# Performance work log

Measured on AMD Instinct MI355X. Metric: run time of the kernel, lower is better.

The kernel has to match this reference:

```python
import jax, jax.numpy as jnp
import numpy as np

H = 32        # query heads
KVH = 8       # kv heads
HD = 64       # head_dim
N_REP = H // KVH
THETA = 10000.0


def _rope_cos_sin(seq_len, dim):
    # freqs_cis[t, i] = exp(1j * t * theta^{-2i/dim}) -> return cos, sin [S, dim//2]
    inv_freq = 1.0 / (THETA ** (jnp.arange(0, dim, 2, dtype=jnp.float32) / dim))
    t = jnp.arange(seq_len, dtype=jnp.float32)
    freqs = jnp.outer(t, inv_freq)  # [S, dim//2]
    return jnp.cos(freqs), jnp.sin(freqs)


def _apply_rope(x, cos, sin):
    # x: [B, S, h, HD]; pairs are interleaved (even=real, odd=imag)
    xr = x[..., 0::2]
    xi = x[..., 1::2]
    c = cos[None, :, None, :]
    s = sin[None, :, None, :]
    out_r = xr * c - xi * s
    out_i = xr * s + xi * c
    return jnp.stack([out_r, out_i], axis=-1).reshape(x.shape)


def setup_inputs() -> dict:
    key = jax.random.key(0)
    ks = jax.random.split(key, 5)
    D = 2048
    B, S = 1, 2048
    scale = 0.02
    return {
        "hidden_states": jax.random.normal(ks[0], (B, S, D), jnp.float32),
        "Wq": jax.random.normal(ks[1], (D, H * HD), jnp.float32) * scale,
        "Wk": jax.random.normal(ks[2], (D, KVH * HD), jnp.float32) * scale,
        "Wv": jax.random.normal(ks[3], (D, KVH * HD), jnp.float32) * scale,
        "Wo": jax.random.normal(ks[4], (H * HD, D), jnp.float32) * scale,
    }


def reference(hidden_states, Wq, Wk, Wv, Wo):
    B, S, D = hidden_states.shape
    xq = (hidden_states @ Wq).reshape(B, S, H, HD)
    xk = (hidden_states @ Wk).reshape(B, S, KVH, HD)
    xv = (hidden_states @ Wv).reshape(B, S, KVH, HD)

    cos, sin = _rope_cos_sin(S, HD)
    xq = _apply_rope(xq, cos, sin)
    xk = _apply_rope(xk, cos, sin)

    # GQA: expand kv heads (kv head g -> query heads g*N_REP .. g*N_REP+N_REP-1)
    keys = jnp.repeat(xk, N_REP, axis=2)    # [B, S, H, HD]
    values = jnp.repeat(xv, N_REP, axis=2)

    q = xq.transpose(0, 2, 1, 3)      # [B, H, S, HD]
    k = keys.transpose(0, 2, 1, 3)
    v = values.transpose(0, 2, 1, 3)

    scores = jnp.einsum('bhqd,bhkd->bhqk', q, k) / jnp.sqrt(jnp.float32(HD))
    causal = jnp.tril(jnp.ones((S, S), dtype=bool))
    scores = jnp.where(causal[None, None], scores, jnp.float32(-jnp.inf))
    probs = jax.nn.softmax(scores.astype(jnp.float32), axis=-1).astype(q.dtype)

    out = jnp.einsum('bhqk,bhkd->bhqd', probs, v)   # [B, H, S, HD]
    out = out.transpose(0, 2, 1, 3).reshape(B, S, H * HD)
    return out @ Wo
```

## Files before the change

kernel.cpp:

```cpp
#include <hip/hip_runtime.h>


#define NH  32
#define NKV 8

typedef __attribute__((ext_vector_type(8))) __bf16 bf16x8;
typedef __attribute__((ext_vector_type(4))) float  f32x4;

#define SCALE_LOG2 0.18033688011112042f
#define L2_10K_32  0.41524101186098665f

__device__ __forceinline__ void glds16(const __bf16* g, __bf16* l) {
  __builtin_amdgcn_global_load_lds(
      (const __attribute__((address_space(1))) unsigned int*)g,
      (__attribute__((address_space(3))) unsigned int*)l, 16, 0, 0);
}

__device__ __forceinline__ float qmax16(float v) {
  int t;
  t = __builtin_amdgcn_mov_dpp(__builtin_bit_cast(int, v), 0x128, 0xf, 0xf, true);
  v = fmaxf(v, __builtin_bit_cast(float, t));
  t = __builtin_amdgcn_mov_dpp(__builtin_bit_cast(int, v), 0x124, 0xf, 0xf, true);
  v = fmaxf(v, __builtin_bit_cast(float, t));
  t = __builtin_amdgcn_mov_dpp(__builtin_bit_cast(int, v), 0x122, 0xf, 0xf, true);
  v = fmaxf(v, __builtin_bit_cast(float, t));
  t = __builtin_amdgcn_mov_dpp(__builtin_bit_cast(int, v), 0x121, 0xf, 0xf, true);
  v = fmaxf(v, __builtin_bit_cast(float, t));
  return v;
}

__device__ __forceinline__ float pair_swap(float v) {
  int t = __builtin_amdgcn_mov_dpp(__builtin_bit_cast(int, v), 0xB1, 0xf, 0xf, true);
  return __builtin_bit_cast(float, t);
}

__device__ __forceinline__ unsigned pack_bf16(float lo, float hi) {
  union { __bf16 b[2]; unsigned u; } r;
  r.b[0] = (__bf16)lo; r.b[1] = (__bf16)hi;
  return r.u;
}

__global__ void k_prep(const float* __restrict__ hx, const float* __restrict__ Wq,
                       const float* __restrict__ Wk, const float* __restrict__ Wv,
                       const float* __restrict__ Wo, __bf16* __restrict__ Xb,
                       __bf16* __restrict__ Wqkvt, __bf16* __restrict__ Wot) {
  __shared__ float t[32][33];
  const int nt = blockIdx.x, k0 = blockIdx.y * 32;
  const int tx = threadIdx.x, ty = threadIdx.y;
  if (nt >= 160) {
    int c0 = (nt - 160) * 32;
#pragma unroll
    for (int j = 0; j < 4; j++) {
      size_t idx = (size_t)(k0 + ty + j * 8) * 2048 + c0 + tx;
      Xb[idx] = (__bf16)hx[idx];
    }
    return;
  }
  const float* W; int ldW, n0; __bf16* dst;
  if (nt < 64)      { W = Wq; ldW = 2048; dst = Wqkvt;                        n0 = nt * 32; }
  else if (nt < 80) { W = Wk; ldW = 512;  dst = Wqkvt + (size_t)2048 * 2048;  n0 = (nt - 64) * 32; }
  else if (nt < 96) { W = Wv; ldW = 512;  dst = Wqkvt + (size_t)2560 * 2048;  n0 = (nt - 80) * 32; }
  else              { W = Wo; ldW = 2048; dst = Wot;                          n0 = (nt - 96) * 32; }
#pragma unroll
  for (int j = 0; j < 4; j++)
    t[ty + j * 8][tx] = W[(size_t)(k0 + ty + j * 8) * ldW + n0 + tx];
  __syncthreads();
#pragma unroll
  for (int j = 0; j < 4; j++)
    dst[(size_t)(n0 + ty + j * 8) * 2048 + k0 + tx] = (__bf16)t[tx][ty + j * 8];
}

__global__ void k_vtrans_b(const __bf16* __restrict__ V, __bf16* __restrict__ Vt) {
  __shared__ __bf16 t[32][33];
  int c0 = blockIdx.x * 32, s0 = blockIdx.y * 32;
  int tx = threadIdx.x, ty = threadIdx.y;
#pragma unroll
  for (int j = 0; j < 4; j++)
    t[ty + j * 8][tx] = V[(size_t)(s0 + ty + j * 8) * 512 + c0 + tx];
  __syncthreads();
#pragma unroll
  for (int j = 0; j < 4; j++)
    Vt[(size_t)(c0 + ty + j * 8) * 2048 + s0 + tx] = t[tx][ty + j * 8];
}

__global__ __launch_bounds__(256) void k_gemm_qkv(
    const __bf16* __restrict__ A, const __bf16* __restrict__ Bt,
    __bf16* __restrict__ Qb, __bf16* __restrict__ Kb, __bf16* __restrict__ Vb) {
  const int K = 2048;
  __shared__ __bf16 As[64][32];
  __shared__ __bf16 Bs[128][32];
  const int tid = threadIdx.x;
  const int m0 = blockIdx.x * 64, n0 = blockIdx.y * 128;
  const int w = tid >> 6, lane = tid & 63, quad = lane >> 4, lid = lane & 15;
  const int wm = (w & 1) * 32, wn = (w >> 1) * 64;
  const int r0 = tid >> 2;
  const int cg = (((tid & 3) ^ ((tid >> 3) & 3)) * 8);
  const __bf16* Ag = A + (size_t)(m0 + r0) * K + cg;
  const __bf16* Bg = Bt + (size_t)(n0 + r0) * K + cg;
  __bf16* Asl = &As[0][0] + tid * 8;
  __bf16* Bsl = &Bs[0][0] + tid * 8;
  const int csw = ((quad ^ ((lid >> 1) & 3)) * 8);
  f32x4 acc[2][4] = {};
  for (int k0 = 0; k0 < K; k0 += 32) {
    __syncthreads();
    glds16(Ag + k0, Asl);
    glds16(Bg + k0, Bsl);
    glds16(Bg + (size_t)64 * K + k0, Bsl + 2048);
    __syncthreads();
    bf16x8 a[2], b[4];
#pragma unroll
    for (int mt = 0; mt < 2; mt++)
      a[mt] = *(const bf16x8*)(&As[wm + mt * 16 + lid][csw]);
#pragma unroll
    for (int nt = 0; nt < 4; nt++)
      b[nt] = *(const bf16x8*)(&Bs[wn + nt * 16 + lid][csw]);
#pragma unroll
    for (int mt = 0; mt < 2; mt++)
#pragma unroll
      for (int nt = 0; nt < 4; nt++)
        acc[mt][nt] = __builtin_amdgcn_mfma_f32_16x16x32_bf16(
            a[mt], b[nt], acc[mt][nt], 0, 0, 0);
  }
  if (n0 >= 2560) {
#pragma unroll
    for (int mt = 0; mt < 2; mt++)
#pragma unroll
      for (int nt = 0; nt < 4; nt++)
#pragma unroll
        for (int i = 0; i < 4; i++) {
          int mm = m0 + wm + mt * 16 + quad * 4 + i;
          int nn = n0 + wn + nt * 16 + lid - 2560;
          Vb[(size_t)mm * 512 + nn] = (__bf16)acc[mt][nt][i];
        }
  } else {
    const bool isQ = (n0 < 2048);
    const float scale = isQ ? SCALE_LOG2 : 1.0f;
    __bf16* dst = isQ ? Qb : Kb;
    const int ldd = isQ ? 2048 : 512;
    const int noff = isQ ? 0 : 2048;
    const bool odd = lid & 1;
#pragma unroll
    for (int nt = 0; nt < 4; nt++) {
      int nn = n0 + wn + nt * 16 + lid;
      int fi = (nn & 63) >> 1;
      float inv = __builtin_amdgcn_exp2f(-(float)fi * L2_10K_32);
#pragma unroll
      for (int mt = 0; mt < 2; mt++)
#pragma unroll
        for (int i = 0; i < 4; i++) {
          int mm = m0 + wm + mt * 16 + quad * 4 + i;
          float ang = (float)mm * inv;
          float sn, cs;
          __sincosf(ang, &sn, &cs);
          float v = acc[mt][nt][i];
          float p = __shfl_xor(v, 1);
          float o = v * cs + (odd ? p : -p) * sn;
          dst[(size_t)mm * ldd + nn - noff] = (__bf16)(o * scale);
        }
    }
  }
}

__global__ __launch_bounds__(256) void k_gemm_out(
    const __bf16* __restrict__ A, const __bf16* __restrict__ Bt,
    float* __restrict__ C) {
  const int K = 2048, N = 2048;
  __shared__ __bf16 As[64][32];
  __shared__ __bf16 Bs[128][32];
  const int tid = threadIdx.x;
  const int m0 = blockIdx.x * 64, n0 = blockIdx.y * 128;
  const int w = tid >> 6, lane = tid & 63, quad = lane >> 4, lid = lane & 15;
  const int wm = (w & 1) * 32, wn = (w >> 1) * 64;
  const int r0 = tid >> 2;
  const int cg = (((tid & 3) ^ ((tid >> 3) & 3)) * 8);
  const __bf16* Ag = A + (size_t)(m0 + r0) * K + cg;
  const __bf16* Bg = Bt + (size_t)(n0 + r0) * K + cg;
  __bf16* Asl = &As[0][0] + tid * 8;
  __bf16* Bsl = &Bs[0][0] + tid * 8;
  const int csw = ((quad ^ ((lid >> 1) & 3)) * 8);
  f32x4 acc[2][4] = {};
  for (int k0 = 0; k0 < K; k0 += 32) {
    __syncthreads();
    glds16(Ag + k0, Asl);
    glds16(Bg + k0, Bsl);
    glds16(Bg + (size_t)64 * K + k0, Bsl + 2048);
    __syncthreads();
    bf16x8 a[2], b[4];
#pragma unroll
    for (int mt = 0; mt < 2; mt++)
      a[mt] = *(const bf16x8*)(&As[wm + mt * 16 + lid][csw]);
#pragma unroll
    for (int nt = 0; nt < 4; nt++)
      b[nt] = *(const bf16x8*)(&Bs[wn + nt * 16 + lid][csw]);
#pragma unroll
    for (int mt = 0; mt < 2; mt++)
#pragma unroll
      for (int nt = 0; nt < 4; nt++)
        acc[mt][nt] = __builtin_amdgcn_mfma_f32_16x16x32_bf16(
            a[mt], b[nt], acc[mt][nt], 0, 0, 0);
  }
#pragma unroll
  for (int mt = 0; mt < 2; mt++)
#pragma unroll
    for (int nt = 0; nt < 4; nt++)
#pragma unroll
      for (int i = 0; i < 4; i++) {
        int mm = m0 + wm + mt * 16 + quad * 4 + i;
        int nn = n0 + wn + nt * 16 + lid;
        C[(size_t)mm * N + nn] = acc[mt][nt][i];
      }
}

__global__ __launch_bounds__(256) void k_attn(
    const __bf16* __restrict__ Q, const __bf16* __restrict__ Kc,
    const __bf16* __restrict__ Vt, __bf16* __restrict__ Oc) {
  __shared__ char smem[51200];
  __bf16* PsB = (__bf16*)smem;
  __bf16* QsB = (__bf16*)smem;
  __bf16* KsB = (__bf16*)(smem + 18432);
  __bf16* VsB = (__bf16*)(smem + 34816);
  const int h = blockIdx.x;
  const int qt = 15 - blockIdx.y;
  const int q0 = qt * 128;
  const int nkv = 2 * qt + 2;
  const int kvh = h >> 2;
  const int tid = threadIdx.x;
  const int w = tid >> 6, lane = tid & 63, quad = lane >> 4, lid = lane & 15;
  const int r0 = tid >> 3;
  const int cg0 = (((tid & 7) ^ (r0 & 7)) * 8);

  const __bf16* Qg = Q + (size_t)(q0 + r0) * 2048 + h * 64 + cg0;
  const __bf16* Kg = Kc + kvh * 64 + cg0;
  const __bf16* Vg = Vt + ((size_t)(kvh * 64 + r0)) * 2048 + cg0;

  glds16(Qg,                     QsB + tid * 8);
  glds16(Qg + (size_t)32 * 2048, QsB + (tid + 256) * 8);
  glds16(Qg + (size_t)64 * 2048, QsB + (tid + 512) * 8);
  glds16(Qg + (size_t)96 * 2048, QsB + (tid + 768) * 8);
  glds16(Kg + (size_t)r0 * 512,        KsB + tid * 8);
  glds16(Kg + (size_t)(r0 + 32) * 512, KsB + (tid + 256) * 8);
  glds16(Vg,                     VsB + tid * 8);
  glds16(Vg + (size_t)32 * 2048, VsB + (tid + 256) * 8);
  __syncthreads();

  bf16x8 aq[2][2];
#pragma unroll
  for (int mt = 0; mt < 2; mt++) {
    int row = w * 32 + mt * 16 + lid;
    int cl = (quad ^ (row & 7)) * 8;
    aq[mt][0] = *(const bf16x8*)(QsB + row * 64 + cl);
    aq[mt][1] = *(const bf16x8*)(QsB + row * 64 + (cl ^ 32));
  }
  __syncthreads();

  bf16x8 bone;
#pragma unroll
  for (int j = 0; j < 8; j++) bone[j] = (lid == 0) ? (__bf16)1.0f : (__bf16)0.0f;

  f32x4 Oacc[2][4] = {};
  f32x4 Lacc[2] = {};
  float mi[2][4];
#pragma unroll
  for (int mt = 0; mt < 2; mt++)
#pragma unroll
    for (int i = 0; i < 4; i++) mi[mt][i] = -1e30f;

  for (int kt = 0; kt < nkv; kt++) {
    const int cb = kt & 1;
    if (kt + 1 < nkv) {
      const int nb = cb ^ 1;
      const size_t kv1 = (size_t)(kt + 1) * 64;
      glds16(Kg + (kv1 + r0) * 512,        KsB + nb * 4096 + tid * 8);
      glds16(Kg + (kv1 + r0 + 32) * 512,   KsB + nb * 4096 + (tid + 256) * 8);
      glds16(Vg + kv1,                     VsB + nb * 4096 + tid * 8);
      glds16(Vg + (size_t)32 * 2048 + kv1, VsB + nb * 4096 + (tid + 256) * 8);
    }

    f32x4 Sc[2][4] = {};
#pragma unroll
    for (int nt = 0; nt < 4; nt++) {
      int row = nt * 16 + lid;
      int cl = (quad ^ (lid & 7)) * 8;
      bf16x8 b0 = *(const bf16x8*)(KsB + cb * 4096 + row * 64 + cl);
      bf16x8 b1 = *(const bf16x8*)(KsB + cb * 4096 + row * 64 + (cl ^ 32));
#pragma unroll
      for (int mt = 0; mt < 2; mt++) {
        Sc[mt][nt] = __builtin_amdgcn_mfma_f32_16x16x32_bf16(aq[mt][0], b0, Sc[mt][nt], 0, 0, 0);
        Sc[mt][nt] = __builtin_amdgcn_mfma_f32_16x16x32_bf16(aq[mt][1], b1, Sc[mt][nt], 0, 0, 0);
      }
    }
    if (kt >= nkv - 2) {
#pragma unroll
      for (int mt = 0; mt < 2; mt++)
#pragma unroll
        for (int nt = 0; nt < 4; nt++)
#pragma unroll
          for (int i = 0; i < 4; i++) {
            int kvg = kt * 64 + nt * 16 + lid;
            int qrg = q0 + w * 32 + mt * 16 + quad * 4 + i;
            if (kvg > qrg) Sc[mt][nt][i] = -1e30f;
          }
    }

    float alpha[2][4];
#pragma unroll
    for (int mt = 0; mt < 2; mt++)
#pragma unroll
      for (int i = 0; i < 4; i++) {
        float m = fmaxf(fmaxf(Sc[mt][0][i], Sc[mt][1][i]),
                        fmaxf(Sc[mt][2][i], Sc[mt][3][i]));
        m = qmax16(m);
        float mnew = fmaxf(mi[mt][i], m);
        alpha[mt][i] = __builtin_amdgcn_exp2f(mi[mt][i] - mnew);
        mi[mt][i] = mnew;
      }
#pragma unroll
    for (int mt = 0; mt < 2; mt++)
#pragma unroll
      for (int nt = 0; nt < 4; nt++)
#pragma unroll
        for (int i = 0; i < 4; i++)
          Sc[mt][nt][i] = __builtin_amdgcn_exp2f(Sc[mt][nt][i] - mi[mt][i]);

#pragma unroll
    for (int mt = 0; mt < 2; mt++)
#pragma unroll
      for (int t = 0; t < 2; t++)
#pragma unroll
        for (int i = 0; i < 4; i++) {
          float pA = Sc[mt][2 * t][i], pB = Sc[mt][2 * t + 1][i];
          float send = (lid & 1) ? pA : pB;
          float recv = pair_swap(send);
          float lo = (lid & 1) ? recv : pA;
          float hi = (lid & 1) ? pB : recv;
          int row = mt * 16 + quad * 4 + i;
          int col = t * 32 + ((lid & 1) ? (lid + 15) : lid);
          *(unsigned*)(PsB + (size_t)w * 2304 + row * 72 + col) = pack_bf16(lo, hi);
        }

#pragma unroll
    for (int mt = 0; mt < 2; mt++) {
#pragma unroll
      for (int nt = 0; nt < 4; nt++)
#pragma unroll
        for (int i = 0; i < 4; i++) Oacc[mt][nt][i] *= alpha[mt][i];
#pragma unroll
      for (int i = 0; i < 4; i++) Lacc[mt][i] *= alpha[mt][i];
    }

#pragma unroll
    for (int kc = 0; kc < 2; kc++) {
      bf16x8 ap[2];
#pragma unroll
      for (int mt = 0; mt < 2; mt++)
        ap[mt] = *(const bf16x8*)(PsB + (size_t)w * 2304 + (mt * 16 + lid) * 72 +
                                  kc * 32 + quad * 8);
#pragma unroll
      for (int mt = 0; mt < 2; mt++)
        Lacc[mt] = __builtin_amdgcn_mfma_f32_16x16x32_bf16(ap[mt], bone, Lacc[mt], 0, 0, 0);
#pragma unroll
      for (int nt = 0; nt < 4; nt++) {
        int row = nt * 16 + lid;
        int cl = (((kc * 4 + quad) ^ (lid & 7)) * 8);
        bf16x8 bv = *(const bf16x8*)(VsB + cb * 4096 + row * 64 + cl);
#pragma unroll
        for (int mt = 0; mt < 2; mt++)
          Oacc[mt][nt] = __builtin_amdgcn_mfma_f32_16x16x32_bf16(ap[mt], bv, Oacc[mt][nt], 0, 0, 0);
      }
    }
    __syncthreads();
  }

#pragma unroll
  for (int mt = 0; mt < 2; mt++)
#pragma unroll
    for (int i = 0; i < 4; i++) {
      float li = __shfl(Lacc[mt][i], lane & 48);
      float r = 1.0f / li;
#pragma unroll
      for (int nt = 0; nt < 4; nt++) {
        int qrow = q0 + w * 32 + mt * 16 + quad * 4 + i;
        int hd = nt * 16 + lid;
        Oc[(size_t)qrow * 2048 + h * 64 + hd] = (__bf16)(Oacc[mt][nt][i] * r);
      }
    }
}

extern "C" void kernel_launch(void* const* d_in, const int* in_sizes, int n_in,
                              void* d_out, int out_size, void* d_ws, size_t ws_size,
                              hipStream_t stream) {
  const float* hx = (const float*)d_in[0];
  const float* Wq = (const float*)d_in[1];
  const float* Wk = (const float*)d_in[2];
  const float* Wv = (const float*)d_in[3];
  const float* Wo = (const float*)d_in[4];
  float* out = (float*)d_out;

  char* ws = (char*)d_ws;
  size_t off = 0;
  auto alloc = [&](size_t bytes) -> void* {
    void* p = ws + off;
    off += (bytes + 255) & ~(size_t)255;
    return p;
  };
  __bf16* Xb    = (__bf16*)alloc((size_t)2048 * 2048 * 2);
  __bf16* Wqkvt = (__bf16*)alloc((size_t)3072 * 2048 * 2);
  __bf16* Wot   = (__bf16*)alloc((size_t)2048 * 2048 * 2);
  __bf16* Qb    = (__bf16*)alloc((size_t)2048 * 2048 * 2);
  __bf16* Kb    = (__bf16*)alloc((size_t)2048 * 512 * 2);
  __bf16* Vb    = (__bf16*)alloc((size_t)2048 * 512 * 2);
  __bf16* Vtg   = (__bf16*)alloc((size_t)512 * 2048 * 2);
  __bf16* AOb   = (__bf16*)alloc((size_t)2048 * 2048 * 2);

  k_prep<<<dim3(224, 64), dim3(32, 8), 0, stream>>>(hx, Wq, Wk, Wv, Wo,
                                                    Xb, Wqkvt, Wot);
  k_gemm_qkv<<<dim3(32, 24), 256, 0, stream>>>(Xb, Wqkvt, Qb, Kb, Vb);
  k_vtrans_b<<<dim3(16, 64), dim3(32, 8), 0, stream>>>(Vb, Vtg);
  k_attn<<<dim3(NH, 16), 256, 0, stream>>>(Qb, Kb, Vtg, AOb);
  k_gemm_out<<<dim3(32, 16), 256, 0, stream>>>(AOb, Wot, out);
}
```

Before: 238.5 us.

## Split attention KV work across waves, drop online max, vectorize prep transpose

```diff
diff --git a/kernel.cpp b/kernel.cpp
--- a/kernel.cpp
+++ b/kernel.cpp
@@ -5,6 +5,7 @@
 #define NKV 8
 
 typedef __attribute__((ext_vector_type(8))) __bf16 bf16x8;
+typedef __attribute__((ext_vector_type(4))) __bf16 bf16x4;
 typedef __attribute__((ext_vector_type(4))) float  f32x4;
 
 #define SCALE_LOG2 0.18033688011112042f
@@ -16,19 +17,6 @@
       (__attribute__((address_space(3))) unsigned int*)l, 16, 0, 0);
 }
 
-__device__ __forceinline__ float qmax16(float v) {
-  int t;
-  t = __builtin_amdgcn_mov_dpp(__builtin_bit_cast(int, v), 0x128, 0xf, 0xf, true);
-  v = fmaxf(v, __builtin_bit_cast(float, t));
-  t = __builtin_amdgcn_mov_dpp(__builtin_bit_cast(int, v), 0x124, 0xf, 0xf, true);
-  v = fmaxf(v, __builtin_bit_cast(float, t));
-  t = __builtin_amdgcn_mov_dpp(__builtin_bit_cast(int, v), 0x122, 0xf, 0xf, true);
-  v = fmaxf(v, __builtin_bit_cast(float, t));
-  t = __builtin_amdgcn_mov_dpp(__builtin_bit_cast(int, v), 0x121, 0xf, 0xf, true);
-  v = fmaxf(v, __builtin_bit_cast(float, t));
-  return v;
-}
-
 __device__ __forceinline__ float pair_swap(float v) {
   int t = __builtin_amdgcn_mov_dpp(__builtin_bit_cast(int, v), 0xB1, 0xf, 0xf, true);
   return __builtin_bit_cast(float, t);
@@ -40,34 +28,38 @@
   return r.u;
 }
 
-__global__ void k_prep(const float* __restrict__ hx, const float* __restrict__ Wq,
-                       const float* __restrict__ Wk, const float* __restrict__ Wv,
-                       const float* __restrict__ Wo, __bf16* __restrict__ Xb,
-                       __bf16* __restrict__ Wqkvt, __bf16* __restrict__ Wot) {
-  __shared__ float t[32][33];
+__global__ __launch_bounds__(256) void k_prep(
+    const float* __restrict__ hx, const float* __restrict__ Wq,
+    const float* __restrict__ Wk, const float* __restrict__ Wv,
+    const float* __restrict__ Wo, __bf16* __restrict__ Xb,
+    __bf16* __restrict__ Wqkvt, __bf16* __restrict__ Wot) {
+  __shared__ float t[32 * 36];
   const int nt = blockIdx.x, k0 = blockIdx.y * 32;
-  const int tx = threadIdx.x, ty = threadIdx.y;
+  const int tid = threadIdx.x;
+  const int r = tid >> 3, c4 = (tid & 7) * 4;
   if (nt >= 160) {
     int c0 = (nt - 160) * 32;
-#pragma unroll
-    for (int j = 0; j < 4; j++) {
-      size_t idx = (size_t)(k0 + ty + j * 8) * 2048 + c0 + tx;
-      Xb[idx] = (__bf16)hx[idx];
-    }
+    float4 v = *(const float4*)(hx + (size_t)(k0 + r) * 2048 + c0 + c4);
+    bf16x4 o;
+    o[0] = (__bf16)v.x; o[1] = (__bf16)v.y; o[2] = (__bf16)v.z; o[3] = (__bf16)v.w;
+    *(bf16x4*)(Xb + (size_t)(k0 + r) * 2048 + c0 + c4) = o;
     return;
   }
   const float* W; int ldW, n0; __bf16* dst;
-  if (nt < 64)      { W = Wq; ldW = 2048; dst = Wqkvt;                        n0 = nt * 32; }
-  else if (nt < 80) { W = Wk; ldW = 512;  dst = Wqkvt + (size_t)2048 * 2048;  n0 = (nt - 64) * 32; }
-  else if (nt < 96) { W = Wv; ldW = 512;  dst = Wqkvt + (size_t)2560 * 2048;  n0 = (nt - 80) * 32; }
-  else              { W = Wo; ldW = 2048; dst = Wot;                          n0 = (nt - 96) * 32; }
-#pragma unroll
-  for (int j = 0; j < 4; j++)
-    t[ty + j * 8][tx] = W[(size_t)(k0 + ty + j * 8) * ldW + n0 + tx];
+  if (nt < 64)      { W = Wq; ldW = 2048; dst = Wqkvt;                       n0 = nt * 32; }
+  else if (nt < 80) { W = Wk; ldW = 512;  dst = Wqkvt + (size_t)2048 * 2048; n0 = (nt - 64) * 32; }
+  else if (nt < 96) { W = Wv; ldW = 512;  dst = Wqkvt + (size_t)2560 * 2048; n0 = (nt - 80) * 32; }
+  else              { W = Wo; ldW = 2048; dst = Wot;                         n0 = (nt - 96) * 32; }
+  float4 v = *(const float4*)(W + (size_t)(k0 + r) * ldW + n0 + c4);
+  *(float4*)(t + r * 36 + ((((c4 >> 2) ^ r) & 7) << 2)) = v;
   __syncthreads();
-#pragma unroll
-  for (int j = 0; j < 4; j++)
-    dst[(size_t)(n0 + ty + j * 8) * 2048 + k0 + tx] = (__bf16)t[tx][ty + j * 8];
+  bf16x4 o;
+#pragma unroll
+  for (int j = 0; j < 4; j++) {
+    int kk = c4 + j;
+    o[j] = (__bf16)t[kk * 36 + ((((r >> 2) ^ kk) & 7) << 2) + (r & 3)];
+  }
+  *(bf16x4*)(dst + (size_t)(n0 + r) * 2048 + k0 + c4) = o;
 }
 
 __global__ void k_vtrans_b(const __bf16* __restrict__ V, __bf16* __restrict__ Vt) {
@@ -211,179 +203,145 @@
       }
 }
 
-__global__ __launch_bounds__(256) void k_attn(
+__global__ __launch_bounds__(256, 4) void k_attn(
     const __bf16* __restrict__ Q, const __bf16* __restrict__ Kc,
     const __bf16* __restrict__ Vt, __bf16* __restrict__ Oc) {
-  __shared__ char smem[51200];
-  __bf16* PsB = (__bf16*)smem;
-  __bf16* QsB = (__bf16*)smem;
-  __bf16* KsB = (__bf16*)(smem + 18432);
-  __bf16* VsB = (__bf16*)(smem + 34816);
+  __shared__ char smem[26624];
+  __bf16* KsB = (__bf16*)smem;
+  __bf16* VsB = (__bf16*)(smem + 8192);
+  __bf16* PsB = (__bf16*)(smem + 16384);
+  float*  OL  = (float*)smem;
+  float*  Lsh = (float*)(smem + 17408);
   const int h = blockIdx.x;
-  const int qt = 15 - blockIdx.y;
-  const int q0 = qt * 128;
-  const int nkv = 2 * qt + 2;
+  const int qt = 31 - blockIdx.y;
+  const int q0 = qt * 64;
   const int kvh = h >> 2;
   const int tid = threadIdx.x;
   const int w = tid >> 6, lane = tid & 63, quad = lane >> 4, lid = lane & 15;
+  const int qh = w & 1, kh = w >> 1;
   const int r0 = tid >> 3;
   const int cg0 = (((tid & 7) ^ (r0 & 7)) * 8);
 
-  const __bf16* Qg = Q + (size_t)(q0 + r0) * 2048 + h * 64 + cg0;
+  bf16x8 aq[2][2];
+#pragma unroll
+  for (int mt = 0; mt < 2; mt++)
+#pragma unroll
+    for (int ks = 0; ks < 2; ks++)
+      aq[mt][ks] = *(const bf16x8*)(
+          Q + (size_t)(q0 + qh * 32 + mt * 16 + lid) * 2048 + h * 64 +
+          ks * 32 + quad * 8);
+
+  bf16x8 bone;
+#pragma unroll
+  for (int j = 0; j < 8; j++) bone[j] = (lid == 0) ? (__bf16)1.0f : (__bf16)0.0f;
+
   const __bf16* Kg = Kc + kvh * 64 + cg0;
   const __bf16* Vg = Vt + ((size_t)(kvh * 64 + r0)) * 2048 + cg0;
-
-  glds16(Qg,                     QsB + tid * 8);
-  glds16(Qg + (size_t)32 * 2048, QsB + (tid + 256) * 8);
-  glds16(Qg + (size_t)64 * 2048, QsB + (tid + 512) * 8);
-  glds16(Qg + (size_t)96 * 2048, QsB + (tid + 768) * 8);
-  glds16(Kg + (size_t)r0 * 512,        KsB + tid * 8);
-  glds16(Kg + (size_t)(r0 + 32) * 512, KsB + (tid + 256) * 8);
-  glds16(Vg,                     VsB + tid * 8);
-  glds16(Vg + (size_t)32 * 2048, VsB + (tid + 256) * 8);
-  __syncthreads();
-
-  bf16x8 aq[2][2];
-#pragma unroll
-  for (int mt = 0; mt < 2; mt++) {
-    int row = w * 32 + mt * 16 + lid;
-    int cl = (quad ^ (row & 7)) * 8;
-    aq[mt][0] = *(const bf16x8*)(QsB + row * 64 + cl);
-    aq[mt][1] = *(const bf16x8*)(QsB + row * 64 + (cl ^ 32));
-  }
-  __syncthreads();
-
-  bf16x8 bone;
-#pragma unroll
-  for (int j = 0; j < 8; j++) bone[j] = (lid == 0) ? (__bf16)1.0f : (__bf16)0.0f;
+  __bf16* Pw = PsB + w * 1280;
 
   f32x4 Oacc[2][4] = {};
   f32x4 Lacc[2] = {};
-  float mi[2][4];
-#pragma unroll
-  for (int mt = 0; mt < 2; mt++)
-#pragma unroll
-    for (int i = 0; i < 4; i++) mi[mt][i] = -1e30f;
-
-  for (int kt = 0; kt < nkv; kt++) {
-    const int cb = kt & 1;
-    if (kt + 1 < nkv) {
-      const int nb = cb ^ 1;
-      const size_t kv1 = (size_t)(kt + 1) * 64;
-      glds16(Kg + (kv1 + r0) * 512,        KsB + nb * 4096 + tid * 8);
-      glds16(Kg + (kv1 + r0 + 32) * 512,   KsB + nb * 4096 + (tid + 256) * 8);
-      glds16(Vg + kv1,                     VsB + nb * 4096 + tid * 8);
-      glds16(Vg + (size_t)32 * 2048 + kv1, VsB + nb * 4096 + (tid + 256) * 8);
-    }
-
-    f32x4 Sc[2][4] = {};
-#pragma unroll
-    for (int nt = 0; nt < 4; nt++) {
-      int row = nt * 16 + lid;
+
+  for (int kt = 0; kt <= qt; kt++) {
+    const int kv0 = kt * 64;
+    glds16(Kg + (size_t)(kv0 + r0) * 512,        KsB + tid * 8);
+    glds16(Kg + (size_t)(kv0 + r0 + 32) * 512,   KsB + (tid + 256) * 8);
+    glds16(Vg + kv0,                             VsB + tid * 8);
+    glds16(Vg + (size_t)32 * 2048 + kv0,         VsB + (tid + 256) * 8);
+    __syncthreads();
+
+    f32x4 Sc[2][2] = {};
+#pragma unroll
+    for (int nt = 0; nt < 2; nt++) {
+      int krow = kh * 32 + nt * 16 + lid;
       int cl = (quad ^ (lid & 7)) * 8;
-      bf16x8 b0 = *(const bf16x8*)(KsB + cb * 4096 + row * 64 + cl);
-      bf16x8 b1 = *(const bf16x8*)(KsB + cb * 4096 + row * 64 + (cl ^ 32));
+      bf16x8 b0 = *(const bf16x8*)(KsB + krow * 64 + cl);
+      bf16x8 b1 = *(const bf16x8*)(KsB + krow * 64 + (cl ^ 32));
 #pragma unroll
       for (int mt = 0; mt < 2; mt++) {
         Sc[mt][nt] = __builtin_amdgcn_mfma_f32_16x16x32_bf16(aq[mt][0], b0, Sc[mt][nt], 0, 0, 0);
         Sc[mt][nt] = __builtin_amdgcn_mfma_f32_16x16x32_bf16(aq[mt][1], b1, Sc[mt][nt], 0, 0, 0);
       }
     }
-    if (kt >= nkv - 2) {
+    if (kt == qt) {
 #pragma unroll
       for (int mt = 0; mt < 2; mt++)
 #pragma unroll
-        for (int nt = 0; nt < 4; nt++)
+        for (int nt = 0; nt < 2; nt++)
 #pragma unroll
           for (int i = 0; i < 4; i++) {
-            int kvg = kt * 64 + nt * 16 + lid;
-            int qrg = q0 + w * 32 + mt * 16 + quad * 4 + i;
+            int kvg = kv0 + kh * 32 + nt * 16 + lid;
+            int qrg = q0 + qh * 32 + mt * 16 + quad * 4 + i;
             if (kvg > qrg) Sc[mt][nt][i] = -1e30f;
           }
     }
 
-    float alpha[2][4];
 #pragma unroll
     for (int mt = 0; mt < 2; mt++)
 #pragma unroll
       for (int i = 0; i < 4; i++) {
-        float m = fmaxf(fmaxf(Sc[mt][0][i], Sc[mt][1][i]),
-                        fmaxf(Sc[mt][2][i], Sc[mt][3][i]));
-        m = qmax16(m);
-        float mnew = fmaxf(mi[mt][i], m);
-        alpha[mt][i] = __builtin_amdgcn_exp2f(mi[mt][i] - mnew);
-        mi[mt][i] = mnew;
+        float pA = __builtin_amdgcn_exp2f(Sc[mt][0][i]);
+        float pB = __builtin_amdgcn_exp2f(Sc[mt][1][i]);
+        float send = (lid & 1) ? pA : pB;
+        float recv = pair_swap(send);
+        float lo = (lid & 1) ? recv : pA;
+        float hi = (lid & 1) ? pB : recv;
+        int row = mt * 16 + quad * 4 + i;
+        int col = (lid & 1) ? (lid + 15) : lid;
+        *(unsigned*)(Pw + row * 40 + col) = pack_bf16(lo, hi);
       }
+
+    bf16x8 ap[2];
+#pragma unroll
+    for (int mt = 0; mt < 2; mt++)
+      ap[mt] = *(const bf16x8*)(Pw + (mt * 16 + lid) * 40 + quad * 8);
+#pragma unroll
+    for (int mt = 0; mt < 2; mt++)
+      Lacc[mt] = __builtin_amdgcn_mfma_f32_16x16x32_bf16(ap[mt], bone, Lacc[mt], 0, 0, 0);
+#pragma unroll
+    for (int nt = 0; nt < 4; nt++) {
+      bf16x8 bv = *(const bf16x8*)(
+          VsB + (nt * 16 + lid) * 64 + (((kh * 4 + quad) ^ (lid & 7)) * 8));
+#pragma unroll
+      for (int mt = 0; mt < 2; mt++)
+        Oacc[mt][nt] = __builtin_amdgcn_mfma_f32_16x16x32_bf16(ap[mt], bv, Oacc[mt][nt], 0, 0, 0);
+    }
+    __syncthreads();
+  }
+
+  if (kh == 1) {
 #pragma unroll
     for (int mt = 0; mt < 2; mt++)
 #pragma unroll
       for (int nt = 0; nt < 4; nt++)
 #pragma unroll
         for (int i = 0; i < 4; i++)
-          Sc[mt][nt][i] = __builtin_amdgcn_exp2f(Sc[mt][nt][i] - mi[mt][i]);
-
-#pragma unroll
-    for (int mt = 0; mt < 2; mt++)
-#pragma unroll
-      for (int t = 0; t < 2; t++)
-#pragma unroll
-        for (int i = 0; i < 4; i++) {
-          float pA = Sc[mt][2 * t][i], pB = Sc[mt][2 * t + 1][i];
-          float send = (lid & 1) ? pA : pB;
-          float recv = pair_swap(send);
-          float lo = (lid & 1) ? recv : pA;
-          float hi = (lid & 1) ? pB : recv;
-          int row = mt * 16 + quad * 4 + i;
-          int col = t * 32 + ((lid & 1) ? (lid + 15) : lid);
-          *(unsigned*)(PsB + (size_t)w * 2304 + row * 72 + col) = pack_bf16(lo, hi);
+          OL[qh * 2176 + (mt * 16 + quad * 4 + i) * 68 + nt * 16 + lid] =
+              Oacc[mt][nt][i];
+    if (lid == 0)
+#pragma unroll
+      for (int mt = 0; mt < 2; mt++)
+#pragma unroll
+        for (int i = 0; i < 4; i++)
+          Lsh[qh * 32 + mt * 16 + quad * 4 + i] = Lacc[mt][i];
+  }
+  __syncthreads();
+  if (kh == 0) {
+#pragma unroll
+    for (int mt = 0; mt < 2; mt++)
+#pragma unroll
+      for (int i = 0; i < 4; i++) {
+        int row = mt * 16 + quad * 4 + i;
+        float lsum = __shfl(Lacc[mt][i], lane & 48) + Lsh[qh * 32 + row];
+        float rs = 1.0f / lsum;
+#pragma unroll
+        for (int nt = 0; nt < 4; nt++) {
+          float o = Oacc[mt][nt][i] + OL[qh * 2176 + row * 68 + nt * 16 + lid];
+          Oc[(size_t)(q0 + qh * 32 + row) * 2048 + h * 64 + nt * 16 + lid] =
+              (__bf16)(o * rs);
         }
-
-#pragma unroll
-    for (int mt = 0; mt < 2; mt++) {
-#pragma unroll
-      for (int nt = 0; nt < 4; nt++)
-#pragma unroll
-        for (int i = 0; i < 4; i++) Oacc[mt][nt][i] *= alpha[mt][i];
-#pragma unroll
-      for (int i = 0; i < 4; i++) Lacc[mt][i] *= alpha[mt][i];
-    }
-
-#pragma unroll
-    for (int kc = 0; kc < 2; kc++) {
-      bf16x8 ap[2];
-#pragma unroll
-      for (int mt = 0; mt < 2; mt++)
-        ap[mt] = *(const bf16x8*)(PsB + (size_t)w * 2304 + (mt * 16 + lid) * 72 +
-                                  kc * 32 + quad * 8);
-#pragma unroll
-      for (int mt = 0; mt < 2; mt++)
-        Lacc[mt] = __builtin_amdgcn_mfma_f32_16x16x32_bf16(ap[mt], bone, Lacc[mt], 0, 0, 0);
-#pragma unroll
-      for (int nt = 0; nt < 4; nt++) {
-        int row = nt * 16 + lid;
-        int cl = (((kc * 4 + quad) ^ (lid & 7)) * 8);
-        bf16x8 bv = *(const bf16x8*)(VsB + cb * 4096 + row * 64 + cl);
-#pragma unroll
-        for (int mt = 0; mt < 2; mt++)
-          Oacc[mt][nt] = __builtin_amdgcn_mfma_f32_16x16x32_bf16(ap[mt], bv, Oacc[mt][nt], 0, 0, 0);
       }
-    }
-    __syncthreads();
-  }
-
-#pragma unroll
-  for (int mt = 0; mt < 2; mt++)
-#pragma unroll
-    for (int i = 0; i < 4; i++) {
-      float li = __shfl(Lacc[mt][i], lane & 48);
-      float r = 1.0f / li;
-#pragma unroll
-      for (int nt = 0; nt < 4; nt++) {
-        int qrow = q0 + w * 32 + mt * 16 + quad * 4 + i;
-        int hd = nt * 16 + lid;
-        Oc[(size_t)qrow * 2048 + h * 64 + hd] = (__bf16)(Oacc[mt][nt][i] * r);
-      }
-    }
+  }
 }
 
 extern "C" void kernel_launch(void* const* d_in, const int* in_sizes, int n_in,
@@ -412,10 +370,9 @@
   __bf16* Vtg   = (__bf16*)alloc((size_t)512 * 2048 * 2);
   __bf16* AOb   = (__bf16*)alloc((size_t)2048 * 2048 * 2);
 
-  k_prep<<<dim3(224, 64), dim3(32, 8), 0, stream>>>(hx, Wq, Wk, Wv, Wo,
-                                                    Xb, Wqkvt, Wot);
+  k_prep<<<dim3(224, 64), 256, 0, stream>>>(hx, Wq, Wk, Wv, Wo, Xb, Wqkvt, Wot);
   k_gemm_qkv<<<dim3(32, 24), 256, 0, stream>>>(Xb, Wqkvt, Qb, Kb, Vb);
   k_vtrans_b<<<dim3(16, 64), dim3(32, 8), 0, stream>>>(Vb, Vtg);
-  k_attn<<<dim3(NH, 16), 256, 0, stream>>>(Qb, Kb, Vtg, AOb);
+  k_attn<<<dim3(NH, 32), 256, 0, stream>>>(Qb, Kb, Vtg, AOb);
   k_gemm_out<<<dim3(32, 16), 256, 0, stream>>>(AOb, Wot, out);
 }
```

Result: faster. 216.4 us (-9.2%).
